# Optimization experiments

Hardware: AMD Instinct MI355X
Metric: run time of the kernel (lower is better)

The kernel has to match this reference:

```python
import jax, jax.numpy as jnp
import numpy as np

B, N, D, H = 2, 2048, 512, 8
HD = D // H


def setup_inputs() -> dict:
    key = jax.random.key(0)
    ks = jax.random.split(key, 12)
    s = 1.0 / np.sqrt(D)
    inp = {
        "x": jax.random.normal(ks[0], (B, N, D), dtype=jnp.float32),
        "adjacency": jax.random.randint(ks[1], (B, N, N), 0, 2, dtype=jnp.int32),
        "Wq": jax.random.uniform(ks[2], (D, D), jnp.float32, -s, s),
        "bq": jnp.zeros((D,), jnp.float32),
        "Wk": jax.random.uniform(ks[3], (D, D), jnp.float32, -s, s),
        "bk": jnp.zeros((D,), jnp.float32),
        "Wv": jax.random.uniform(ks[4], (D, D), jnp.float32, -s, s),
        "bv": jnp.zeros((D,), jnp.float32),
        "Wo": jax.random.uniform(ks[5], (D, D), jnp.float32, -s, s),
        "bo": jnp.zeros((D,), jnp.float32),
        "gamma": jnp.ones((D,), jnp.float32),
        "beta": jnp.zeros((D,), jnp.float32),
    }
    return inp


def reference(x, adjacency, Wq, bq, Wk, bk, Wv, bv, Wo, bo, gamma, beta):
    scale = HD ** -0.5
    # projections -> [B, H, N, HD]
    def proj(W, b):
        return (x @ W.T + b).reshape(B, N, H, HD).transpose(0, 2, 1, 3)
    q = proj(Wq, bq)
    k = proj(Wk, bk)
    v = proj(Wv, bv)
    # [B, H, N, N] attention scores
    scores = jnp.einsum("bhqd,bhkd->bhqk", q, k) * scale
    mask = (adjacency[:, None, :, :] != 0)  # [B, 1->H, N, N]
    scores = jnp.where(mask, scores, -jnp.inf)
    attn = jax.nn.softmax(scores, axis=-1)
    # dropout is identity in eval mode
    ctx = jnp.einsum("bhqk,bhkd->bhqd", attn, v)
    ctx = ctx.transpose(0, 2, 1, 3).reshape(B, N, D)
    out = ctx @ Wo.T + bo
    y = x + out
    mu = jnp.mean(y, axis=-1, keepdims=True)
    var = jnp.var(y, axis=-1, keepdims=True)
    return (y - mu) * jax.lax.rsqrt(var + 1e-5) * gamma + beta
```

## Files before the change

kernel.cpp:

```cpp
#include <hip/hip_runtime.h>
#include <hip/hip_bf16.h>

#define B_  2
#define N_  2048
#define D_  512
#define H_  8
#define HD_ 64

typedef float  f4  __attribute__((ext_vector_type(4)));
typedef int    i4  __attribute__((ext_vector_type(4)));
typedef short  bf16x8 __attribute__((ext_vector_type(8)));
typedef float  f32x4  __attribute__((ext_vector_type(4)));
typedef unsigned short u16x8 __attribute__((ext_vector_type(8)));
typedef unsigned short u16x4 __attribute__((ext_vector_type(4)));

static __device__ __forceinline__ unsigned short f2bf(float f) {
    union { float f; unsigned int u; } v; v.f = f;
    unsigned int r = v.u + 0x7fffu + ((v.u >> 16) & 1u);
    return (unsigned short)(r >> 16);
}

__global__ __launch_bounds__(256) void prep_kernel(
    const float* __restrict__ x,
    const float* __restrict__ Wq, const float* __restrict__ Wk,
    const float* __restrict__ Wv, const float* __restrict__ Wo,
    unsigned short* __restrict__ xh, unsigned short* __restrict__ WhAll)
{
    const size_t e = ((size_t)blockIdx.x * 256 + threadIdx.x) * 8;
    const float* src;
    unsigned short* dst;
    if (e < 2097152) {
        src = x + e;  dst = xh + e;
    } else {
        const size_t e2 = e - 2097152;
        const int wi = (int)(e2 >> 18);
        const size_t off = e2 & 262143;
        const float* Ws = (wi == 0) ? Wq : (wi == 1) ? Wk : (wi == 2) ? Wv : Wo;
        src = Ws + off;  dst = WhAll + (size_t)wi * 262144 + off;
    }
    f4 a = *(const f4*)src;
    f4 b = *(const f4*)(src + 4);
    u16x8 o;
    #pragma unroll
    for (int j = 0; j < 4; ++j) { o[j] = f2bf(a[j]); o[j + 4] = f2bf(b[j]); }
    *(u16x8*)dst = o;
}

template <int OUT_MODE>
__device__ __forceinline__ void mfma_gemm_body(
    const unsigned short* __restrict__ Ah, const unsigned short* __restrict__ Wh,
    const float* __restrict__ bias, float* __restrict__ outf,
    unsigned short* __restrict__ outh, int r0, int c0)
{
    __shared__ unsigned short Asm[128][72];
    __shared__ unsigned short Bsm[128][72];

    const int tid  = threadIdx.x;
    const int lane = tid & 63;
    const int w    = tid >> 6;
    const int wr   = w >> 1, wc = w & 1;
    const int l15  = lane & 15, lhi = lane >> 4;

    f32x4 acc[4][4];
    #pragma unroll
    for (int mi = 0; mi < 4; ++mi)
        #pragma unroll
        for (int ni = 0; ni < 4; ++ni)
            acc[mi][ni] = (f32x4){0.f, 0.f, 0.f, 0.f};

    for (int kt = 0; kt < 512; kt += 64) {
        __syncthreads();
        #pragma unroll
        for (int i = 0; i < 4; ++i) {
            const int v   = tid + i * 256;
            const int row = v >> 3;
            const int c8  = (v & 7) * 8;
            *(u16x8*)&Asm[row][c8] =
                *(const u16x8*)&Ah[(size_t)(r0 + row) * 512 + kt + c8];
            *(u16x8*)&Bsm[row][c8] =
                *(const u16x8*)&Wh[(size_t)(c0 + row) * 512 + kt + c8];
        }
        __syncthreads();

        #pragma unroll
        for (int ks = 0; ks < 2; ++ks) {
            bf16x8 a[4], bb[4];
            #pragma unroll
            for (int mi = 0; mi < 4; ++mi)
                a[mi] = *(const bf16x8*)&Asm[wr * 64 + mi * 16 + l15][ks * 32 + lhi * 8];
            #pragma unroll
            for (int ni = 0; ni < 4; ++ni)
                bb[ni] = *(const bf16x8*)&Bsm[wc * 64 + ni * 16 + l15][ks * 32 + lhi * 8];
            #pragma unroll
            for (int mi = 0; mi < 4; ++mi)
                #pragma unroll
                for (int ni = 0; ni < 4; ++ni)
                    acc[mi][ni] = __builtin_amdgcn_mfma_f32_16x16x32_bf16(
                        a[mi], bb[ni], acc[mi][ni], 0, 0, 0);
        }
    }

    #pragma unroll
    for (int ni = 0; ni < 4; ++ni) {
        const int c = c0 + wc * 64 + ni * 16 + l15;
        const float bias_c = bias[c];
        #pragma unroll
        for (int mi = 0; mi < 4; ++mi) {
            #pragma unroll
            for (int reg = 0; reg < 4; ++reg) {
                const int r = r0 + wr * 64 + mi * 16 + lhi * 4 + reg;
                const float vv = acc[mi][ni][reg] + bias_c;
                if (OUT_MODE == 0) {
                    outf[(size_t)r * 512 + c] = vv;
                } else {
                    const int bbn = r >> 11, n = r & (N_ - 1);
                    const int h = c >> 6, hd = c & 63;
                    outh[(((size_t)(bbn * H_ + h)) * N_ + n) * HD_ + hd] = f2bf(vv);
                }
            }
        }
    }
}

__global__ __launch_bounds__(256) void qkv_mfma_kernel(
    const unsigned short* __restrict__ xh, const unsigned short* __restrict__ WhAll,
    const float* __restrict__ bq, const float* __restrict__ bk,
    const float* __restrict__ bv,
    unsigned short* __restrict__ Qh, unsigned short* __restrict__ Kh,
    unsigned short* __restrict__ Vh)
{
    const int z = blockIdx.z;
    const unsigned short* Wh = WhAll + (size_t)z * 262144;
    const float* bias = (z == 0) ? bq : (z == 1) ? bk : bv;
    unsigned short* dst = (z == 0) ? Qh : (z == 1) ? Kh : Vh;
    mfma_gemm_body<1>(xh, Wh, bias, nullptr, dst,
                      blockIdx.y * 128, blockIdx.x * 128);
}

__global__ __launch_bounds__(256) void wo_mfma_kernel(
    const unsigned short* __restrict__ ctxh, const unsigned short* __restrict__ WhAll,
    const float* __restrict__ bo, float* __restrict__ y1)
{
    mfma_gemm_body<0>(ctxh, WhAll + 3 * 262144, bo, y1, nullptr,
                      blockIdx.y * 128, blockIdx.x * 128);
}

__global__ __launch_bounds__(256) void attn_kernel(
    const unsigned short* __restrict__ Q, const unsigned short* __restrict__ K,
    const unsigned short* __restrict__ V, const int* __restrict__ adj,
    unsigned short* __restrict__ ctxh)
{
    __shared__ unsigned short K_lds[64][72];
    __shared__ unsigned short Vt_lds[64][72];
    __shared__ unsigned short P_lds[4][16][72];
    __shared__ float fac_lds[4][16];

    const int tid  = threadIdx.x;
    const int lane = tid & 63;
    const int w    = tid >> 6;
    const int l15  = lane & 15, lhi = lane >> 4;
    const int bh = blockIdx.y;
    const int b  = bh >> 3;
    const int hh = bh & 7;
    const int q0 = blockIdx.x * 64;

    const unsigned short* Qbh = Q + (size_t)bh * N_ * HD_;
    const unsigned short* Kbh = K + (size_t)bh * N_ * HD_;
    const unsigned short* Vbh = V + (size_t)bh * N_ * HD_;
    const int* adjb = adj + (size_t)b * N_ * N_;

    const int qrow = q0 + w * 16 + l15;
    bf16x8 aq0 = *(const bf16x8*)&Qbh[(size_t)qrow * HD_ + lhi * 8];
    bf16x8 aq1 = *(const bf16x8*)&Qbh[(size_t)qrow * HD_ + 32 + lhi * 8];

    const int qrow_base = q0 + w * 16 + lhi * 4;

    f32x4 acc[4];
    #pragma unroll
    for (int t = 0; t < 4; ++t) acc[t] = (f32x4){0.f, 0.f, 0.f, 0.f};
    float m_q = -__builtin_inff();
    float l_q = 0.0f;
    const float NEG_INF = -__builtin_inff();
    const float scale = 0.125f;

    i4 adjc[4], adjn[4];
    #pragma unroll
    for (int kt = 0; kt < 4; ++kt)
        adjc[kt] = *(const i4*)&adjb[(size_t)qrow * N_ + kt * 16 + lhi * 4];

    for (int kc = 0; kc < N_; kc += 64) {
        __syncthreads();

        {
            const int k  = tid & 63;
            const int c2 = tid >> 6;
            u16x8 k0 = *(const u16x8*)&Kbh[(size_t)(kc + k) * HD_ + c2 * 8];
            u16x8 k1 = *(const u16x8*)&Kbh[(size_t)(kc + k) * HD_ + (c2 + 4) * 8];
            *(u16x8*)&K_lds[k][c2 * 8]       = k0;
            *(u16x8*)&K_lds[k][(c2 + 4) * 8] = k1;
        }
        {
            const int k2  = (tid & 31) * 2;
            const int dvb = (tid >> 5) * 8;
            u16x8 v0 = *(const u16x8*)&Vbh[(size_t)(kc + k2) * HD_ + dvb];
            u16x8 v1 = *(const u16x8*)&Vbh[(size_t)(kc + k2 + 1) * HD_ + dvb];
            #pragma unroll
            for (int i = 0; i < 8; ++i) {
                unsigned int pair = (unsigned int)(unsigned short)v0[i] |
                                    ((unsigned int)(unsigned short)v1[i] << 16);
                *(unsigned int*)&Vt_lds[dvb + i][k2] = pair;
            }
        }

        const int kcn = (kc + 64) & (N_ - 1);
        #pragma unroll
        for (int kt = 0; kt < 4; ++kt)
            adjn[kt] = *(const i4*)&adjb[(size_t)qrow * N_ + kcn + kt * 16 + lhi * 4];

        __syncthreads();

        f32x4 s[4];
        #pragma unroll
        for (int kt = 0; kt < 4; ++kt) {
            bf16x8 bk0 = *(const bf16x8*)&K_lds[kt * 16 + l15][lhi * 8];
            bf16x8 bk1 = *(const bf16x8*)&K_lds[kt * 16 + l15][32 + lhi * 8];
            f32x4 z = {0.f, 0.f, 0.f, 0.f};
            z = __builtin_amdgcn_mfma_f32_16x16x32_bf16(bk0, aq0, z, 0, 0, 0);
            s[kt] = __builtin_amdgcn_mfma_f32_16x16x32_bf16(bk1, aq1, z, 0, 0, 0);
        }

        float sm[16];
        #pragma unroll
        for (int kt = 0; kt < 4; ++kt)
            #pragma unroll
            for (int r = 0; r < 4; ++r)
                sm[kt * 4 + r] = adjc[kt][r] ? s[kt][r] * scale : NEG_INF;

        float mx = sm[0];
        #pragma unroll
        for (int i = 1; i < 16; ++i) mx = fmaxf(mx, sm[i]);
        mx = fmaxf(mx, __shfl_xor(mx, 16));
        mx = fmaxf(mx, __shfl_xor(mx, 32));

        const float mnew = fmaxf(m_q, mx);
        float fac, p[16];
        if (mnew == NEG_INF) {
            fac = 1.0f;
            #pragma unroll
            for (int i = 0; i < 16; ++i) p[i] = 0.0f;
        } else {
            fac = __expf(m_q - mnew);
            #pragma unroll
            for (int i = 0; i < 16; ++i)
                p[i] = __expf(sm[i] - mnew);
        }
        m_q = mnew;

        float rs = 0.0f;
        #pragma unroll
        for (int i = 0; i < 16; ++i) rs += p[i];
        rs += __shfl_xor(rs, 16);
        rs += __shfl_xor(rs, 32);
        l_q = l_q * fac + rs;

        if (lhi == 0) fac_lds[w][l15] = fac;
        f4 fac4 = *(const f4*)&fac_lds[w][lhi * 4];
        #pragma unroll
        for (int t = 0; t < 4; ++t)
            #pragma unroll
            for (int r = 0; r < 4; ++r)
                acc[t][r] *= fac4[r];

        #pragma unroll
        for (int kt = 0; kt < 4; ++kt) {
            u16x4 pw;
            #pragma unroll
            for (int r = 0; r < 4; ++r) pw[r] = f2bf(p[kt * 4 + r]);
            *(u16x4*)&P_lds[w][l15][kt * 16 + lhi * 4] = pw;
        }

        #pragma unroll
        for (int ks = 0; ks < 2; ++ks) {
            bf16x8 ap = *(const bf16x8*)&P_lds[w][l15][ks * 32 + lhi * 8];
            #pragma unroll
            for (int dvt = 0; dvt < 4; ++dvt) {
                bf16x8 bv = *(const bf16x8*)&Vt_lds[dvt * 16 + l15][ks * 32 + lhi * 8];
                acc[dvt] = __builtin_amdgcn_mfma_f32_16x16x32_bf16(ap, bv, acc[dvt], 0, 0, 0);
            }
        }

        #pragma unroll
        for (int kt = 0; kt < 4; ++kt) adjc[kt] = adjn[kt];
    }

    if (lhi == 0) fac_lds[w][l15] = l_q;
    f4 lv = *(const f4*)&fac_lds[w][lhi * 4];
    #pragma unroll
    for (int r = 0; r < 4; ++r) {
        const int q = qrow_base + r;
        const float inv = (lv[r] > 0.0f) ? 1.0f / lv[r] : 0.0f;
        #pragma unroll
        for (int dvt = 0; dvt < 4; ++dvt)
            ctxh[((size_t)(b * N_ + q)) * D_ + hh * HD_ + dvt * 16 + l15] =
                f2bf(acc[dvt][r] * inv);
    }
}

__global__ __launch_bounds__(64) void ln_kernel(
    const float* __restrict__ x, const float* __restrict__ y1,
    const float* __restrict__ gamma, const float* __restrict__ beta,
    float* __restrict__ out)
{
    const int row = blockIdx.x;
    const int tid = threadIdx.x;
    const size_t base = (size_t)row * 512 + tid * 8;

    f4 v0 = *(const f4*)&x[base]     + *(const f4*)&y1[base];
    f4 v1 = *(const f4*)&x[base + 4] + *(const f4*)&y1[base + 4];

    float s = v0[0] + v0[1] + v0[2] + v0[3] + v1[0] + v1[1] + v1[2] + v1[3];
    #pragma unroll
    for (int off = 1; off < 64; off <<= 1) s += __shfl_xor(s, off);
    const float mu = s * (1.0f / 512.0f);

    float d2 = 0.0f;
    #pragma unroll
    for (int j = 0; j < 4; ++j) {
        const float a = v0[j] - mu, bq = v1[j] - mu;
        d2 += a * a + bq * bq;
    }
    #pragma unroll
    for (int off = 1; off < 64; off <<= 1) d2 += __shfl_xor(d2, off);
    const float rstd = rsqrtf(d2 * (1.0f / 512.0f) + 1e-5f);

    f4 g0 = *(const f4*)&gamma[tid * 8];
    f4 g1 = *(const f4*)&gamma[tid * 8 + 4];
    f4 be0 = *(const f4*)&beta[tid * 8];
    f4 be1 = *(const f4*)&beta[tid * 8 + 4];
    f4 o0, o1;
    #pragma unroll
    for (int j = 0; j < 4; ++j) {
        o0[j] = (v0[j] - mu) * rstd * g0[j] + be0[j];
        o1[j] = (v1[j] - mu) * rstd * g1[j] + be1[j];
    }
    *(f4*)&out[base]     = o0;
    *(f4*)&out[base + 4] = o1;
}

extern "C" void kernel_launch(void* const* d_in, const int* in_sizes, int n_in,
                              void* d_out, int out_size, void* d_ws, size_t ws_size,
                              hipStream_t stream)
{
    const float* x     = (const float*)d_in[0];
    const int*   adj   = (const int*)  d_in[1];
    const float* Wq    = (const float*)d_in[2];
    const float* bq    = (const float*)d_in[3];
    const float* Wk    = (const float*)d_in[4];
    const float* bk    = (const float*)d_in[5];
    const float* Wv    = (const float*)d_in[6];
    const float* bv    = (const float*)d_in[7];
    const float* Wo    = (const float*)d_in[8];
    const float* bo    = (const float*)d_in[9];
    const float* gamma = (const float*)d_in[10];
    const float* beta  = (const float*)d_in[11];
    float* out = (float*)d_out;

    const size_t elems = (size_t)B_ * N_ * D_;
    unsigned short* Qh    = (unsigned short*)d_ws;
    unsigned short* Kh    = Qh   + elems;
    unsigned short* Vh    = Kh   + elems;
    unsigned short* ctxh  = Vh   + elems;
    unsigned short* xh    = ctxh + elems;
    unsigned short* WhAll = xh   + elems;
    float* y1 = (float*)Qh;

    prep_kernel<<<1536, 256, 0, stream>>>(x, Wq, Wk, Wv, Wo, xh, WhAll);

    qkv_mfma_kernel<<<dim3(4, 32, 3), 256, 0, stream>>>(
        xh, WhAll, bq, bk, bv, Qh, Kh, Vh);

    attn_kernel<<<dim3(N_ / 64, B_ * H_), 256, 0, stream>>>(Qh, Kh, Vh, adj, ctxh);

    wo_mfma_kernel<<<dim3(4, 32), 256, 0, stream>>>(ctxh, WhAll, bo, y1);

    ln_kernel<<<B_ * N_, 64, 0, stream>>>(x, y1, gamma, beta, out);
}
```

Measured before the change: 225.6 us.

## Double-buffer K/V tiles in attention with register prefetch of next chunk

The attention kernel now keeps two LDS buffers for the K and transposed V tiles. At the start of each iteration it issues global loads for the next chunk into registers, and writes them to the other buffer after the current chunk's MFMA work. This cuts the per-iteration barriers from two to one and lets global load latency overlap with compute. In exchange it doubles LDS use for K and V and raises register pressure, which could lower occupancy.

```diff
diff --git a/kernel.cpp b/kernel.cpp
--- a/kernel.cpp
+++ b/kernel.cpp
@@ -150,8 +150,8 @@
     const unsigned short* __restrict__ V, const int* __restrict__ adj,
     unsigned short* __restrict__ ctxh)
 {
-    __shared__ unsigned short K_lds[64][72];
-    __shared__ unsigned short Vt_lds[64][72];
+    __shared__ unsigned short K_lds[2][64][72];
+    __shared__ unsigned short Vt_lds[2][64][72];
     __shared__ unsigned short P_lds[4][16][72];
     __shared__ float fac_lds[4][16];
 
@@ -169,6 +169,11 @@
     const unsigned short* Vbh = V + (size_t)bh * N_ * HD_;
     const int* adjb = adj + (size_t)b * N_ * N_;
 
+    const int sk  = tid & 63;
+    const int sc2 = tid >> 6;
+    const int sv_k2  = (tid & 31) * 2;
+    const int sv_dvb = (tid >> 5) * 8;
+
     const int qrow = q0 + w * 16 + l15;
     bf16x8 aq0 = *(const bf16x8*)&Qbh[(size_t)qrow * HD_ + lhi * 8];
     bf16x8 aq1 = *(const bf16x8*)&Qbh[(size_t)qrow * HD_ + 32 + lhi * 8];
@@ -183,47 +188,42 @@
     const float NEG_INF = -__builtin_inff();
     const float scale = 0.125f;
 
+    {
+        u16x8 k0 = *(const u16x8*)&Kbh[(size_t)sk * HD_ + sc2 * 8];
+        u16x8 k1 = *(const u16x8*)&Kbh[(size_t)sk * HD_ + (sc2 + 4) * 8];
+        *(u16x8*)&K_lds[0][sk][sc2 * 8]       = k0;
+        *(u16x8*)&K_lds[0][sk][(sc2 + 4) * 8] = k1;
+        u16x8 v0 = *(const u16x8*)&Vbh[(size_t)sv_k2 * HD_ + sv_dvb];
+        u16x8 v1 = *(const u16x8*)&Vbh[(size_t)(sv_k2 + 1) * HD_ + sv_dvb];
+        #pragma unroll
+        for (int i = 0; i < 8; ++i) {
+            unsigned int pair = (unsigned int)(unsigned short)v0[i] |
+                                ((unsigned int)(unsigned short)v1[i] << 16);
+            *(unsigned int*)&Vt_lds[0][sv_dvb + i][sv_k2] = pair;
+        }
+    }
     i4 adjc[4], adjn[4];
     #pragma unroll
     for (int kt = 0; kt < 4; ++kt)
         adjc[kt] = *(const i4*)&adjb[(size_t)qrow * N_ + kt * 16 + lhi * 4];
-
+    __syncthreads();
+
+    int cur = 0;
     for (int kc = 0; kc < N_; kc += 64) {
-        __syncthreads();
-
-        {
-            const int k  = tid & 63;
-            const int c2 = tid >> 6;
-            u16x8 k0 = *(const u16x8*)&Kbh[(size_t)(kc + k) * HD_ + c2 * 8];
-            u16x8 k1 = *(const u16x8*)&Kbh[(size_t)(kc + k) * HD_ + (c2 + 4) * 8];
-            *(u16x8*)&K_lds[k][c2 * 8]       = k0;
-            *(u16x8*)&K_lds[k][(c2 + 4) * 8] = k1;
-        }
-        {
-            const int k2  = (tid & 31) * 2;
-            const int dvb = (tid >> 5) * 8;
-            u16x8 v0 = *(const u16x8*)&Vbh[(size_t)(kc + k2) * HD_ + dvb];
-            u16x8 v1 = *(const u16x8*)&Vbh[(size_t)(kc + k2 + 1) * HD_ + dvb];
-            #pragma unroll
-            for (int i = 0; i < 8; ++i) {
-                unsigned int pair = (unsigned int)(unsigned short)v0[i] |
-                                    ((unsigned int)(unsigned short)v1[i] << 16);
-                *(unsigned int*)&Vt_lds[dvb + i][k2] = pair;
-            }
-        }
-
         const int kcn = (kc + 64) & (N_ - 1);
+        u16x8 nk0 = *(const u16x8*)&Kbh[(size_t)(kcn + sk) * HD_ + sc2 * 8];
+        u16x8 nk1 = *(const u16x8*)&Kbh[(size_t)(kcn + sk) * HD_ + (sc2 + 4) * 8];
+        u16x8 nv0 = *(const u16x8*)&Vbh[(size_t)(kcn + sv_k2) * HD_ + sv_dvb];
+        u16x8 nv1 = *(const u16x8*)&Vbh[(size_t)(kcn + sv_k2 + 1) * HD_ + sv_dvb];
         #pragma unroll
         for (int kt = 0; kt < 4; ++kt)
             adjn[kt] = *(const i4*)&adjb[(size_t)qrow * N_ + kcn + kt * 16 + lhi * 4];
 
-        __syncthreads();
-
         f32x4 s[4];
         #pragma unroll
         for (int kt = 0; kt < 4; ++kt) {
-            bf16x8 bk0 = *(const bf16x8*)&K_lds[kt * 16 + l15][lhi * 8];
-            bf16x8 bk1 = *(const bf16x8*)&K_lds[kt * 16 + l15][32 + lhi * 8];
+            bf16x8 bk0 = *(const bf16x8*)&K_lds[cur][kt * 16 + l15][lhi * 8];
+            bf16x8 bk1 = *(const bf16x8*)&K_lds[cur][kt * 16 + l15][32 + lhi * 8];
             f32x4 z = {0.f, 0.f, 0.f, 0.f};
             z = __builtin_amdgcn_mfma_f32_16x16x32_bf16(bk0, aq0, z, 0, 0, 0);
             s[kt] = __builtin_amdgcn_mfma_f32_16x16x32_bf16(bk1, aq1, z, 0, 0, 0);
@@ -284,10 +284,22 @@
             bf16x8 ap = *(const bf16x8*)&P_lds[w][l15][ks * 32 + lhi * 8];
             #pragma unroll
             for (int dvt = 0; dvt < 4; ++dvt) {
-                bf16x8 bv = *(const bf16x8*)&Vt_lds[dvt * 16 + l15][ks * 32 + lhi * 8];
+                bf16x8 bv = *(const bf16x8*)&Vt_lds[cur][dvt * 16 + l15][ks * 32 + lhi * 8];
                 acc[dvt] = __builtin_amdgcn_mfma_f32_16x16x32_bf16(ap, bv, acc[dvt], 0, 0, 0);
             }
         }
+
+        const int nxt = cur ^ 1;
+        *(u16x8*)&K_lds[nxt][sk][sc2 * 8]       = nk0;
+        *(u16x8*)&K_lds[nxt][sk][(sc2 + 4) * 8] = nk1;
+        #pragma unroll
+        for (int i = 0; i < 8; ++i) {
+            unsigned int pair = (unsigned int)(unsigned short)nv0[i] |
+                                ((unsigned int)(unsigned short)nv1[i] << 16);
+            *(unsigned int*)&Vt_lds[nxt][sv_dvb + i][sv_k2] = pair;
+        }
+        __syncthreads();
+        cur = nxt;
 
         #pragma unroll
         for (int kt = 0; kt < 4; ++kt) adjc[kt] = adjn[kt];
```

Measured after the change: 212.1 us. 1.06x faster.
